# Kernel tuning notes

Measured on AMD Instinct MI355X. Metric: run time of the kernel, lower is better.

## Reference

```python
import jax, jax.numpy as jnp
import numpy as np

RHO = 10.0
TAU = 0.1


def setup_inputs() -> dict:
    key = jax.random.key(0)
    k1, k2 = jax.random.split(key)
    N, D, C = 8192, 512, 128
    embeddings = jax.random.normal(k1, (N, D), dtype=jnp.float32)
    classes = jax.random.randint(k2, (N,), 0, C, dtype=jnp.int64)
    return {"embeddings": embeddings, "classes": classes}


def reference(embeddings, classes):
    n = embeddings.shape[0]
    dt = embeddings.dtype

    # calculate_similarities_pt: cosine similarity (dot products of L2-normalized embeddings)
    norms = jnp.linalg.norm(embeddings, axis=1, keepdims=True)
    normed = embeddings / jnp.maximum(norms, jnp.asarray(1e-12, dt))
    dot_products = jnp.einsum("nd,md->nm", normed, normed)  # [N, N]

    # calculate_groups_pt: same-class mask (excluding self) and different-class mask
    eq = classes[:, None] == classes[None, :]
    eye = jnp.eye(n, dtype=bool)
    same_group = (eq & ~eye).astype(dt)       # [N, N]
    different_group = (~eq).astype(dt)        # [N, N]

    # diagonal gets factor -RHO -> strongly negative score, effectively masked out
    raw_scores = ((same_group + different_group) * (1.0 + RHO) - RHO) * dot_products / TAU
    max_raw_score = jnp.max(raw_scores, axis=1, keepdims=True)
    shifted_scores = jnp.exp(raw_scores - max_raw_score)

    shifted_positive_scores = same_group * shifted_scores
    sum_shifted_negative_scores = jnp.sum(different_group * shifted_scores, axis=1, keepdims=True)

    denom = shifted_positive_scores + sum_shifted_negative_scores
    # safe_division: 0 where denominator is 0
    ratio = jnp.where(denom > 0, shifted_positive_scores / jnp.where(denom > 0, denom, 1.0), 0.0)
    # safe_log: 0 where argument is 0 (masked by same_group anyway)
    log_ratio = jnp.where(ratio > 0, jnp.log(jnp.where(ratio > 0, ratio, 1.0)), 0.0)
    infonce_losses = -log_ratio * same_group

    num_pos = jnp.sum(same_group)
    loss = jnp.where(num_pos > 0, jnp.sum(infonce_losses) / jnp.where(num_pos > 0, num_pos, 1.0), 0.0)
    return loss
```

## Files before the change

### kernel.cpp

```cpp
#include <hip/hip_runtime.h>
#include <hip/hip_bf16.h>


constexpr int   D      = 512;
constexpr int   BT     = 128;
constexpr int   BK     = 64;
constexpr int   NSTEP  = D / BK;
constexpr float SHIFT  = 10.0f;
constexpr float QS2    = 10.0f / 16129.0f;

typedef __attribute__((ext_vector_type(4))) int i32x4;
typedef unsigned char uchar;
typedef unsigned long ulong_t;

__device__ inline void gload_lds16(const uchar* g, void* l) {
    __builtin_amdgcn_global_load_lds(
        (const __attribute__((address_space(1))) void*)g,
        (__attribute__((address_space(3))) void*)l, 16, 0, 0);
}

__global__ void k_normalize(const float* __restrict__ emb,
                            const int* __restrict__ classes,
                            uchar* __restrict__ normed,
                            int* __restrict__ hist, int n) {
    if (blockIdx.x == 0) {
        __shared__ int h[128];
        if (threadIdx.x < 128) h[threadIdx.x] = 0;
        __syncthreads();
        for (int i = threadIdx.x; i < n; i += 256)
            atomicAdd(&h[classes[i] & 127], 1);
        __syncthreads();
        if (threadIdx.x < 128) hist[threadIdx.x] = h[threadIdx.x];
    }
    int row  = blockIdx.x * 4 + (threadIdx.x >> 6);
    int lane = threadIdx.x & 63;
    if (row >= n) return;
    const float4* src = (const float4*)(emb + (size_t)row * D);
    float4 a = src[lane * 2];
    float4 b = src[lane * 2 + 1];
    float ss = a.x*a.x + a.y*a.y + a.z*a.z + a.w*a.w
             + b.x*b.x + b.y*b.y + b.z*b.z + b.w*b.w;
#pragma unroll
    for (int m = 1; m < 64; m <<= 1) ss += __shfl_xor(ss, m, 64);
    float sc = 127.0f / fmaxf(sqrtf(ss), 1e-12f);
    union { signed char c[8]; ulong_t u; } o;
    float v[8] = {a.x, a.y, a.z, a.w, b.x, b.y, b.z, b.w};
#pragma unroll
    for (int k = 0; k < 8; ++k) {
        int q = (int)rintf(v[k] * sc);
        q = q > 127 ? 127 : (q < -127 ? -127 : q);
        o.c[k] = (signed char)q;
    }
    *(ulong_t*)&normed[(size_t)row * D + lane * 8] = o.u;
}

__global__ __launch_bounds__(256, 3) void k_zgemm(
    const uchar* __restrict__ normed, const int* __restrict__ classes,
    float* __restrict__ Zpart, int n, int nb, int npairs) {
    __shared__ char ring[3][16384];
    __shared__ int clsrow[BT], clscol[BT];

    const int tid  = threadIdx.x;
    const int lane = tid & 63;
    const int w    = tid >> 6;
    const int wm   = w >> 1, wn = w & 1;
    const int l15  = lane & 15, l4 = lane >> 4;
    const size_t QS = (size_t)64 * n;

    int q8 = npairs >> 3, r8 = npairs & 7;
    int xcd = blockIdx.x & 7, off = blockIdx.x >> 3;
    int orig = (xcd < r8 ? xcd * (q8 + 1) : r8 * (q8 + 1) + (xcd - r8) * q8) + off;

    const int sgrid = nb >> 3;
    int idx = orig, si = 0;
    for (;;) { int rc = 36 + (sgrid - 1 - si) * 64; if (idx < rc) break; idx -= rc; ++si; }
    int bi, bj;
    if (idx < 36) { int u = 0, rem = 8; while (idx >= rem) { idx -= rem; ++u; --rem; }
                    bi = si * 8 + u; bj = si * 8 + u + idx; }
    else { idx -= 36; int sj = si + 1 + (idx >> 6); int v = idx & 63;
           bi = si * 8 + (v >> 3); bj = sj * 8 + (v & 7); }
    const int row0 = bi * BT, c0 = bj * BT;
    const bool diagblk = (bi == bj);

    if (tid < BT) clsrow[tid] = classes[row0 + tid];
    else          clscol[tid - BT] = classes[c0 + tid - BT];
    int crow[16];
#pragma unroll
    for (int t = 0; t < 16; ++t)
        crow[t] = classes[row0 + wm * 64 + (t >> 2) * 16 + l4 * 4 + (t & 3)];

    const int src16 = (lane & 3) ^ ((lane >> 3) & 3);
    size_t gA[2], gB[2]; int lo[2];
#pragma unroll
    for (int it = 0; it < 2; ++it) {
        int chunk = w * 2 + it;
        int row   = chunk * 16 + (lane >> 2);
        gA[it] = (size_t)(row0 + row) * D + src16 * 16;
        gB[it] = (size_t)(c0   + row) * D + src16 * 16;
        lo[it] = chunk * 1024;
    }
    char* ringb = &ring[0][0];

    auto STAGE = [&](int sbo, int kk) {
#pragma unroll
        for (int it = 0; it < 2; ++it) {
            gload_lds16(normed + gA[it] + kk, ringb + sbo + lo[it]);
            gload_lds16(normed + gB[it] + kk, ringb + sbo + 8192 + lo[it]);
        }
    };

    i32x4 acc[4][4];
#pragma unroll
    for (int a = 0; a < 4; ++a)
#pragma unroll
        for (int b = 0; b < 4; ++b) acc[a][b] = (i32x4){0, 0, 0, 0};

    STAGE(0, 0);
    STAGE(16384, BK);
    __builtin_amdgcn_sched_barrier(0);
    asm volatile("s_waitcnt vmcnt(4) lgkmcnt(0)" ::: "memory");
    __builtin_amdgcn_s_barrier();
    __builtin_amdgcn_sched_barrier(0);

    const int rsw = (l15 >> 1) & 3;

#pragma unroll
    for (int kt = 0; kt < NSTEP; ++kt) {
        const int cur = kt % 3;
        if (kt + 2 < NSTEP) STAGE(((kt + 2) % 3) * 16384, (kt + 2) * BK);
        const char* la = ringb + cur * 16384;
        const char* lb = la + 8192;
        i32x4 af[4], bfr[4];
#pragma unroll
        for (int mf = 0; mf < 4; ++mf) {
            int ra = wm * 64 + mf * 16 + l15;
            af[mf] = *(const i32x4*)(la + ra * 64 + ((l4 ^ rsw) << 4));
        }
#pragma unroll
        for (int nf = 0; nf < 4; ++nf) {
            int rb = wn * 64 + nf * 16 + l15;
            bfr[nf] = *(const i32x4*)(lb + rb * 64 + ((l4 ^ rsw) << 4));
        }
        __builtin_amdgcn_s_setprio(1);
#pragma unroll
        for (int mf = 0; mf < 4; ++mf)
#pragma unroll
            for (int nf = 0; nf < 4; ++nf)
                acc[mf][nf] = __builtin_amdgcn_mfma_i32_16x16x64_i8(
                    af[mf], bfr[nf], acc[mf][nf], 0, 0, 0);
        __builtin_amdgcn_s_setprio(0);
        __builtin_amdgcn_sched_barrier(0);
        if (kt + 2 < NSTEP)       asm volatile("s_waitcnt vmcnt(4)" ::: "memory");
        else if (kt + 2 == NSTEP) asm volatile("s_waitcnt vmcnt(0)" ::: "memory");
        if (kt + 1 < NSTEP) {
            __builtin_amdgcn_s_barrier();
            __builtin_amdgcn_sched_barrier(0);
        }
    }
    __syncthreads();

    float cqz[4] = {0,0,0,0}, cqn[4] = {0,0,0,0}, cqp[4] = {0,0,0,0};
    float* redr = (float*)ringb;
    float* redc = (float*)(ringb + 16384);

#pragma unroll
    for (int mf = 0; mf < 4; ++mf) {
#pragma unroll
        for (int r = 0; r < 4; ++r) {
            int rr = wm * 64 + mf * 16 + l4 * 4 + r;
            int rg = row0 + rr;
            int cr = crow[mf * 4 + r];
            float z = 0.f, ns = 0.f, p1 = 0.f;
#pragma unroll
            for (int nf = 0; nf < 4; ++nf) {
                int cc = wn * 64 + nf * 16 + l15;
                float t = fmaf((float)acc[mf][nf][r], QS2, -SHIFT);
                float e = __expf(t);
                bool same = (cr == clscol[cc]);
                bool dg   = (rg == c0 + cc);
                if (!same) { z += e; cqz[nf] += e; }
                else if (!dg) { ns += t; p1 += e; cqn[nf] += t; cqp[nf] += e; }
            }
#pragma unroll
            for (int m = 1; m < 16; m <<= 1) {
                z  += __shfl_xor(z,  m, 16);
                ns += __shfl_xor(ns, m, 16);
                p1 += __shfl_xor(p1, m, 16);
            }
            if (l15 == 0) {
                float* p = &redr[(wn * 128 + rr) * 3];
                p[0] = z; p[1] = ns; p[2] = p1;
            }
        }
    }
    if (!diagblk) {
#pragma unroll
        for (int nf = 0; nf < 4; ++nf) {
            float z = cqz[nf], nsv = cqn[nf], p = cqp[nf];
            z += __shfl_xor(z, 16, 64);  z += __shfl_xor(z, 32, 64);
            nsv += __shfl_xor(nsv, 16, 64); nsv += __shfl_xor(nsv, 32, 64);
            p += __shfl_xor(p, 16, 64);  p += __shfl_xor(p, 32, 64);
            if (l4 == 0) {
                float* pp = &redc[(wm * 128 + wn * 64 + nf * 16 + l15) * 3];
                pp[0] = z; pp[1] = nsv; pp[2] = p;
            }
        }
    }
    __syncthreads();

    if (tid < BT) {
#pragma unroll
        for (int q = 0; q < 3; ++q)
            Zpart[q * QS + (size_t)bj * n + row0 + tid] =
                redr[(0 * 128 + tid) * 3 + q] + redr[(1 * 128 + tid) * 3 + q];
    } else if (!diagblk) {
        int cc = tid - BT;
#pragma unroll
        for (int q = 0; q < 3; ++q)
            Zpart[q * QS + (size_t)bi * n + c0 + cc] =
                redc[(0 * 128 + cc) * 3 + q] + redc[(1 * 128 + cc) * 3 + q];
    }
}

__global__ void k_rowterms(const float* __restrict__ Zpart,
                           const int* __restrict__ classes,
                           const int* __restrict__ hist,
                           float* __restrict__ rowloss,
                           float* __restrict__ rowcnt, int n) {
    int i = blockIdx.x * 256 + threadIdx.x;
    if (i >= n) return;
    const size_t QS = (size_t)64 * n;
    float z = 0.f, ns = 0.f, p1 = 0.f;
    for (int s = 0; s < 64; ++s) {
        size_t o = (size_t)s * n + i;
        z  += Zpart[o];
        ns += Zpart[QS + o];
        p1 += Zpart[2 * QS + o];
    }
    float c = (float)(hist[classes[i] & 127] - 1);
    rowloss[i] = -ns + c * logf(z) + p1 / z;
    rowcnt[i]  = c;
}

__global__ void k_final(const float* __restrict__ rowloss,
                        const float* __restrict__ rowcnt,
                        float* __restrict__ out, int n) {
    __shared__ float sl[1024];
    __shared__ float sc[1024];
    float l = 0.f, c = 0.f;
    for (int i = threadIdx.x; i < n; i += 1024) {
        l += rowloss[i];
        c += rowcnt[i];
    }
    sl[threadIdx.x] = l;
    sc[threadIdx.x] = c;
    __syncthreads();
    for (int s = 512; s > 0; s >>= 1) {
        if (threadIdx.x < s) {
            sl[threadIdx.x] += sl[threadIdx.x + s];
            sc[threadIdx.x] += sc[threadIdx.x + s];
        }
        __syncthreads();
    }
    if (threadIdx.x == 0)
        out[0] = (sc[0] > 0.f) ? sl[0] / sc[0] : 0.f;
}

extern "C" void kernel_launch(void* const* d_in, const int* in_sizes, int n_in,
                              void* d_out, int out_size, void* d_ws, size_t ws_size,
                              hipStream_t stream) {
    const float* emb     = (const float*)d_in[0];
    const int*   classes = (const int*)d_in[1];
    float*       out     = (float*)d_out;
    const int n  = in_sizes[1];
    const int nb = n / BT;
    const int npairs = nb * (nb + 1) / 2;

    uchar*  normed  = (uchar*)d_ws;
    float*  Zpart   = (float*)((char*)d_ws + (size_t)n * D);
    float*  rowloss = Zpart + (size_t)3 * 64 * n;
    float*  rowcnt  = rowloss + n;
    int*    hist    = (int*)(rowcnt + n);

    k_normalize<<<n / 4, 256, 0, stream>>>(emb, classes, normed, hist, n);
    k_zgemm<<<npairs, 256, 0, stream>>>(normed, classes, Zpart, n, nb, npairs);
    k_rowterms<<<(n + 255) / 256, 256, 0, stream>>>(Zpart, classes, hist, rowloss, rowcnt, n);
    k_final<<<1, 1024, 0, stream>>>(rowloss, rowcnt, out, n);
}
```

Measured before the change: 75.84 us.

## Switch GEMM to double-buffered BK=128 pipeline and base-2 exponent scaling

The int8 similarity GEMM now uses a two-stage ring of 32KB buffers with a K step of 128 instead of a three-stage ring with a K step of 64. This halves the number of barrier and wait points and issues more MFMAs per synchronisation. The trade is a larger LDS footprint, so occupancy drops to 2 blocks per CU, and each step waits for all loads (vmcnt(0)) with less prefetch depth. The exponent is also precomputed in base 2 so it uses exp2f, and the positive-term sum is rescaled by ln2 in the row kernel.

```diff
diff --git a/kernel.cpp b/kernel.cpp
--- a/kernel.cpp
+++ b/kernel.cpp
@@ -4,10 +4,11 @@
 
 constexpr int   D      = 512;
 constexpr int   BT     = 128;
-constexpr int   BK     = 64;
+constexpr int   BK     = 128;
 constexpr int   NSTEP  = D / BK;
-constexpr float SHIFT  = 10.0f;
-constexpr float QS2    = 10.0f / 16129.0f;
+constexpr float SHIFTL = 14.4269504088896340f;
+constexpr float QS2L   = 10.0f * 1.4426950408889634f / 16129.0f;
+constexpr float LN2    = 0.6931471805599453f;
 
 typedef __attribute__((ext_vector_type(4))) int i32x4;
 typedef unsigned char uchar;
@@ -54,10 +55,10 @@
     *(ulong_t*)&normed[(size_t)row * D + lane * 8] = o.u;
 }
 
-__global__ __launch_bounds__(256, 3) void k_zgemm(
+__global__ __launch_bounds__(256, 2) void k_zgemm(
     const uchar* __restrict__ normed, const int* __restrict__ classes,
     float* __restrict__ Zpart, int n, int nb, int npairs) {
-    __shared__ char ring[3][16384];
+    __shared__ char ring[2][32768];
     __shared__ int clsrow[BT], clscol[BT];
 
     const int tid  = threadIdx.x;
@@ -103,9 +104,14 @@
 
     auto STAGE = [&](int sbo, int kk) {
 #pragma unroll
-        for (int it = 0; it < 2; ++it) {
-            gload_lds16(normed + gA[it] + kk, ringb + sbo + lo[it]);
-            gload_lds16(normed + gB[it] + kk, ringb + sbo + 8192 + lo[it]);
+        for (int h = 0; h < 2; ++h) {
+            int kh = kk + h * 64;
+            int so = sbo + h * 16384;
+#pragma unroll
+            for (int it = 0; it < 2; ++it) {
+                gload_lds16(normed + gA[it] + kh, ringb + so + lo[it]);
+                gload_lds16(normed + gB[it] + kh, ringb + so + 8192 + lo[it]);
+            }
         }
     };
 
@@ -116,9 +122,8 @@
         for (int b = 0; b < 4; ++b) acc[a][b] = (i32x4){0, 0, 0, 0};
 
     STAGE(0, 0);
-    STAGE(16384, BK);
     __builtin_amdgcn_sched_barrier(0);
-    asm volatile("s_waitcnt vmcnt(4) lgkmcnt(0)" ::: "memory");
+    asm volatile("s_waitcnt vmcnt(0) lgkmcnt(0)" ::: "memory");
     __builtin_amdgcn_s_barrier();
     __builtin_amdgcn_sched_barrier(0);
 
@@ -126,33 +131,38 @@
 
 #pragma unroll
     for (int kt = 0; kt < NSTEP; ++kt) {
-        const int cur = kt % 3;
-        if (kt + 2 < NSTEP) STAGE(((kt + 2) % 3) * 16384, (kt + 2) * BK);
-        const char* la = ringb + cur * 16384;
-        const char* lb = la + 8192;
-        i32x4 af[4], bfr[4];
-#pragma unroll
-        for (int mf = 0; mf < 4; ++mf) {
-            int ra = wm * 64 + mf * 16 + l15;
-            af[mf] = *(const i32x4*)(la + ra * 64 + ((l4 ^ rsw) << 4));
-        }
-#pragma unroll
-        for (int nf = 0; nf < 4; ++nf) {
-            int rb = wn * 64 + nf * 16 + l15;
-            bfr[nf] = *(const i32x4*)(lb + rb * 64 + ((l4 ^ rsw) << 4));
+        const int cur = kt & 1;
+        if (kt + 1 < NSTEP) STAGE((cur ^ 1) * 32768, (kt + 1) * BK);
+        const char* base = ringb + cur * 32768;
+        i32x4 af[2][4], bfr[2][4];
+#pragma unroll
+        for (int h = 0; h < 2; ++h) {
+            const char* la = base + h * 16384;
+            const char* lb = la + 8192;
+#pragma unroll
+            for (int mf = 0; mf < 4; ++mf) {
+                int ra = wm * 64 + mf * 16 + l15;
+                af[h][mf] = *(const i32x4*)(la + ra * 64 + ((l4 ^ rsw) << 4));
+            }
+#pragma unroll
+            for (int nf = 0; nf < 4; ++nf) {
+                int rb = wn * 64 + nf * 16 + l15;
+                bfr[h][nf] = *(const i32x4*)(lb + rb * 64 + ((l4 ^ rsw) << 4));
+            }
         }
         __builtin_amdgcn_s_setprio(1);
 #pragma unroll
-        for (int mf = 0; mf < 4; ++mf)
-#pragma unroll
-            for (int nf = 0; nf < 4; ++nf)
-                acc[mf][nf] = __builtin_amdgcn_mfma_i32_16x16x64_i8(
-                    af[mf], bfr[nf], acc[mf][nf], 0, 0, 0);
+        for (int h = 0; h < 2; ++h)
+#pragma unroll
+            for (int mf = 0; mf < 4; ++mf)
+#pragma unroll
+                for (int nf = 0; nf < 4; ++nf)
+                    acc[mf][nf] = __builtin_amdgcn_mfma_i32_16x16x64_i8(
+                        af[h][mf], bfr[h][nf], acc[mf][nf], 0, 0, 0);
         __builtin_amdgcn_s_setprio(0);
         __builtin_amdgcn_sched_barrier(0);
-        if (kt + 2 < NSTEP)       asm volatile("s_waitcnt vmcnt(4)" ::: "memory");
-        else if (kt + 2 == NSTEP) asm volatile("s_waitcnt vmcnt(0)" ::: "memory");
         if (kt + 1 < NSTEP) {
+            asm volatile("s_waitcnt vmcnt(0)" ::: "memory");
             __builtin_amdgcn_s_barrier();
             __builtin_amdgcn_sched_barrier(0);
         }
@@ -174,8 +184,8 @@
 #pragma unroll
             for (int nf = 0; nf < 4; ++nf) {
                 int cc = wn * 64 + nf * 16 + l15;
-                float t = fmaf((float)acc[mf][nf][r], QS2, -SHIFT);
-                float e = __expf(t);
+                float t = fmaf((float)acc[mf][nf][r], QS2L, -SHIFTL);
+                float e = exp2f(t);
                 bool same = (cr == clscol[cc]);
                 bool dg   = (rg == c0 + cc);
                 if (!same) { z += e; cqz[nf] += e; }
@@ -238,7 +248,7 @@
         p1 += Zpart[2 * QS + o];
     }
     float c = (float)(hist[classes[i] & 127] - 1);
-    rowloss[i] = -ns + c * logf(z) + p1 / z;
+    rowloss[i] = -ns * LN2 + c * logf(z) + p1 / z;
     rowcnt[i]  = c;
 }
 
```

New measurement: 89.13 us. 1.18x slower.
